# Performance work log

Measured on AMD Instinct MI355X. Metric: run time of the kernel, lower is better.

The kernel has to match this reference:

```python
import jax, jax.numpy as jnp
import numpy as np

EPS = 1e-5  # BatchNorm3d default eps


def conv1x1(x, w, b):
    # x: (b, cin, t, h, w); w: (cout, cin); b: (cout,)
    return jnp.einsum('bcthw,oc->bothw', x, w) + b[None, :, None, None, None]


def batchnorm(x):
    # BatchNorm3d(affine=False), training mode: per-channel batch stats over (B,T,H,W)
    mean = jnp.mean(x, axis=(0, 2, 3, 4), keepdims=True)
    var = jnp.var(x, axis=(0, 2, 3, 4), keepdims=True)
    return (x - mean) * jax.lax.rsqrt(var + EPS)


def setup_inputs() -> dict:
    key = jax.random.key(0)
    ks = jax.random.split(key, 9)
    B, C, T, H, W = 4, 512, 16, 14, 14
    IC = C // 4
    s_in = 1.0 / np.sqrt(C)
    s_up = 1.0 / np.sqrt(IC)
    return {
        'maps':    jax.random.normal(ks[0], (B, C, T, H, W), jnp.float32),
        'w_theta': jax.random.uniform(ks[1], (IC, C), jnp.float32, -s_in, s_in),
        'b_theta': jax.random.uniform(ks[2], (IC,),   jnp.float32, -s_in, s_in),
        'w_phalt': jax.random.uniform(ks[3], (IC, C), jnp.float32, -s_in, s_in),
        'b_phalt': jax.random.uniform(ks[4], (IC,),   jnp.float32, -s_in, s_in),
        'w_glob':  jax.random.uniform(ks[5], (IC, C), jnp.float32, -s_in, s_in),
        'b_glob':  jax.random.uniform(ks[6], (IC,),   jnp.float32, -s_in, s_in),
        'w_up':    jax.random.uniform(ks[7], (C, IC), jnp.float32, -s_up, s_up),
        'b_up':    jax.random.uniform(ks[8], (C,),    jnp.float32, -s_up, s_up),
    }


def reference(maps, w_theta, b_theta, w_phalt, b_phalt, w_glob, b_glob, w_up, b_up):
    b, c, t, h, w = maps.shape
    ic = c // 4
    n = t * h * w

    theta_maps = batchnorm(conv1x1(maps, w_theta, b_theta))   # (b, ic, t, h, w)
    phalt_maps = batchnorm(conv1x1(maps, w_phalt, b_phalt))   # computed but UNUSED (bug in original)
    global_maps = batchnorm(conv1x1(maps, w_glob, b_glob))

    theta_x = theta_maps.reshape(b, ic, n)                    # (b, ic, n)
    # NOTE: original code uses theta_maps for phalt_x (faithful to source bug)
    relation = jnp.einsum('bcn,bcm->bnm', theta_x, theta_x)   # (b, n, n)
    relation_normalize = jax.nn.softmax(relation / n, axis=-1)

    global_x = global_maps.reshape(b, ic, n)                  # (b, ic, n)
    y = jnp.einsum('bnm,bcm->bcn', relation_normalize, global_x)
    y = y.reshape(b, ic, t, h, w)

    out = conv1x1(y, w_up, b_up) + maps
    return out
```

## Files before the change

kernel.cpp:

```cpp
#include <hip/hip_runtime.h>
#include <hip/hip_bf16.h>


typedef __attribute__((ext_vector_type(8))) short bf16x8;
typedef __attribute__((ext_vector_type(4))) float f32x4;
typedef __attribute__((ext_vector_type(16))) float f32x16;
typedef __attribute__((ext_vector_type(4))) short s16x4;

#define NTOK 3136
#define NELEM 1605632
#define NSPLIT 4

__device__ inline float bf2f(short u) {
    union { unsigned int i; float f; } v;
    v.i = ((unsigned int)(unsigned short)u) << 16;
    return v.f;
}
__device__ inline short f2bf(float x) {
    union { float f; unsigned int i; } v;
    v.f = x;
    unsigned int r = v.i + 0x7FFFu + ((v.i >> 16) & 1u);
    return (short)(r >> 16);
}
__device__ inline unsigned pk2(float lo, float hi) {
    union { float f; unsigned u; } a, b;
    a.f = lo; b.f = hi;
    return __builtin_amdgcn_perm(b.u, a.u, 0x07060302u);
}
__device__ inline void pl32swap(unsigned &a, unsigned &b) {
    asm("v_permlane32_swap_b32 %0, %1" : "+v"(a), "+v"(b));
}
__device__ inline void glds16(const void* g, void* l) {
    __builtin_amdgcn_global_load_lds((const __attribute__((address_space(1))) void*)g,
                                     (__attribute__((address_space(3))) void*)l, 16, 0, 0);
}

__global__ __launch_bounds__(256) void prep_w(const float* __restrict__ wt,
                                              const float* __restrict__ wg,
                                              const float* __restrict__ wup,
                                              short* __restrict__ Wb,
                                              short* __restrict__ wupb)
{
    const int i = blockIdx.x * 256 + threadIdx.x;
    if (i < 131072) {
        const int r = i >> 9;
        const int c = i & 511;
        const float w = (r < 128) ? wt[(size_t)r * 512 + c] : wg[(size_t)(r - 128) * 512 + c];
        Wb[i] = f2bf(w);
    } else {
        const int j = i - 131072;
        wupb[j] = f2bf(wup[j]);
    }
}

__global__ __launch_bounds__(256) void conv_in_f(const float* __restrict__ maps,
                                                 const short* __restrict__ Wb,
                                                 short* __restrict__ Tt,
                                                 short* __restrict__ Gpre,
                                                 float* __restrict__ psum,
                                                 float* __restrict__ psq)
{
    const int nt = blockIdx.x, b = blockIdx.y;
    const int n0 = nt * 32;
    const int t = threadIdx.x;
    const int w = __builtin_amdgcn_readfirstlane(t >> 6);
    const int lane = t & 63;
    const int l15 = lane & 15, lhi = lane >> 4;

    __shared__ short Bt[32][136];

    const float* mp = maps + (size_t)b * 512 * NTOK + n0;
    const int cl = t >> 3;
    const int f4 = t & 7;

    f32x4 acc[4][2];
#pragma unroll
    for (int g = 0; g < 4; g++)
#pragma unroll
        for (int j = 0; j < 2; j++) acc[g][j] = f32x4{0.f, 0.f, 0.f, 0.f};

    f32x4 rg[4];
#pragma unroll
    for (int p = 0; p < 4; p++)
        rg[p] = *(const f32x4*)(mp + (size_t)(p * 32 + cl) * NTOK + f4 * 4);

    for (int kc = 0; kc < 4; kc++) {
        __syncthreads();
#pragma unroll
        for (int p = 0; p < 4; p++) {
            const int cc = p * 32 + cl;
#pragma unroll
            for (int i = 0; i < 4; i++) Bt[f4 * 4 + i][cc] = f2bf(rg[p][i]);
        }
        if (kc < 3) {
#pragma unroll
            for (int p = 0; p < 4; p++)
                rg[p] = *(const f32x4*)(mp + (size_t)((kc + 1) * 128 + p * 32 + cl) * NTOK + f4 * 4);
        }
        __syncthreads();
#pragma unroll
        for (int ks = 0; ks < 4; ks++) {
            bf16x8 af[4], bv[2];
#pragma unroll
            for (int g = 0; g < 4; g++)
                af[g] = *(const bf16x8*)(Wb + (size_t)(w * 64 + g * 16 + l15) * 512 + kc * 128 + ks * 32 + lhi * 8);
#pragma unroll
            for (int j = 0; j < 2; j++)
                bv[j] = *(const bf16x8*)(&Bt[j * 16 + l15][ks * 32 + lhi * 8]);
#pragma unroll
            for (int g = 0; g < 4; g++)
#pragma unroll
                for (int j = 0; j < 2; j++)
                    acc[g][j] = __builtin_amdgcn_mfma_f32_16x16x32_bf16(af[g], bv[j], acc[g][j], 0, 0, 0);
        }
    }

    if (w < 2) {
#pragma unroll
        for (int g = 0; g < 4; g++)
#pragma unroll
            for (int j = 0; j < 2; j++) {
                s16x4 v;
#pragma unroll
                for (int r = 0; r < 4; r++) v[r] = f2bf(acc[g][j][r]);
                *(s16x4*)(Tt + ((size_t)b * NTOK + n0 + j * 16 + l15) * 128 + w * 64 + g * 16 + lhi * 4) = v;
            }
    } else {
#pragma unroll
        for (int g = 0; g < 4; g++)
#pragma unroll
            for (int j = 0; j < 2; j++)
#pragma unroll
                for (int r = 0; r < 4; r++) {
                    const int icg = (w - 2) * 64 + g * 16 + lhi * 4 + r;
                    Gpre[((size_t)b * 128 + icg) * NTOK + n0 + j * 16 + l15] = f2bf(acc[g][j][r]);
                }
    }
#pragma unroll
    for (int g = 0; g < 4; g++)
#pragma unroll
        for (int r = 0; r < 4; r++) {
            float s = acc[g][0][r] + acc[g][1][r];
            float q = acc[g][0][r] * acc[g][0][r] + acc[g][1][r] * acc[g][1][r];
#pragma unroll
            for (int off = 1; off < 16; off <<= 1) {
                s += __shfl_xor(s, off);
                q += __shfl_xor(q, off);
            }
            if (l15 == 0) {
                const int ch = w * 64 + g * 16 + lhi * 4 + r;
                psum[(size_t)ch * 392 + b * 98 + nt] = s;
                psq [(size_t)ch * 392 + b * 98 + nt] = q;
            }
        }
}

__global__ __launch_bounds__(64) void stats_fin(const float* __restrict__ psum,
                                                const float* __restrict__ psq,
                                                float* __restrict__ st)
{
    const int ch = blockIdx.x;
    const int lane = threadIdx.x;
    float s = 0.f, q = 0.f;
    for (int i = lane; i < 392; i += 64) {
        s += psum[(size_t)ch * 392 + i];
        q += psq [(size_t)ch * 392 + i];
    }
#pragma unroll
    for (int off = 32; off; off >>= 1) { s += __shfl_xor(s, off); q += __shfl_xor(q, off); }
    if (lane == 0) {
        const float mean = s / 12544.f;
        const float var = q / 12544.f - mean * mean;
        st[ch] = mean;
        st[256 + ch] = rsqrtf(var + 1e-5f);
    }
}

__global__ __launch_bounds__(256, 2) void attn_k(const short* __restrict__ Tt,
                                                 const short* __restrict__ Gpre,
                                                 const float* __restrict__ st,
                                                 short* __restrict__ Opart,
                                                 float* __restrict__ dpart)
{
    constexpr int N = NTOK;
    const int b = blockIdx.y, s = blockIdx.z;
    const int w = __builtin_amdgcn_readfirstlane(threadIdx.x >> 6);
    const int lane = threadIdx.x & 63;
    const int l31 = lane & 31, hi = lane >> 5;
    const int q0w = blockIdx.x * 128 + w * 32;

    __shared__ __align__(16) short Kl[2][64][128];
    __shared__ __align__(16) short Vl[2][128][64];

    const short* tb = Tt + (size_t)b * N * 128;
    const short* gb = Gpre + (size_t)b * 128 * N;

    const float kexp = 1.44269504089f / (float)N;
    bf16x8 qf[8];
    {
        int row = q0w + l31; row = row < N ? row : N - 1;
        const short* qp = tb + (size_t)row * 128;
#pragma unroll
        for (int ks = 0; ks < 8; ks++) {
            const int c0 = ks * 16 + hi * 8;
            const bf16x8 v = *(const bf16x8*)(qp + c0);
            const f32x4 mA = *(const f32x4*)(st + c0);
            const f32x4 mB = *(const f32x4*)(st + c0 + 4);
            const f32x4 rA = *(const f32x4*)(st + 256 + c0);
            const f32x4 rB = *(const f32x4*)(st + 256 + c0 + 4);
            bf16x8 q;
#pragma unroll
            for (int j = 0; j < 4; j++) q[j] = f2bf((bf2f(v[j]) - mA[j]) * (rA[j] * rA[j] * kexp));
#pragma unroll
            for (int j = 0; j < 4; j++) q[4 + j] = f2bf((bf2f(v[4 + j]) - mB[j]) * (rB[j] * rB[j] * kexp));
            qf[ks] = q;
        }
    }

    f32x16 accv[4];
#pragma unroll
    for (int it = 0; it < 4; it++)
#pragma unroll
        for (int r = 0; r < 16; r++) accv[it][r] = 0.f;
    float denom = 0.f;

    auto STAGE = [&](int bufi, int m0) {
#pragma unroll
        for (int i = 0; i < 4; i++) {
            const int rb = w * 16 + i * 4;
            const int krow = rb + (lane >> 4);
            const int ls = (lane & 15) ^ (krow & 7);
            glds16(tb + (size_t)(m0 + krow) * 128 + ls * 8, (void*)&Kl[bufi][rb][0]);
        }
#pragma unroll
        for (int i = 0; i < 4; i++) {
            const int rb = w * 32 + i * 8;
            const int vrow = rb + (lane >> 3);
            const int ls = (lane & 7) ^ (vrow & 7);
            glds16(gb + (size_t)vrow * N + m0 + ls * 8, (void*)&Vl[bufi][rb][0]);
        }
    };

    const int nt = (49 - s + NSPLIT - 1) / NSPLIT;
    int mt = s;
    STAGE(0, mt * 64);
    __syncthreads();
    int buf = 0;

    const int fr = (l31 & 7) << 4;

    auto mkpa = [&](const f32x16 &sv, bf16x8 *dst) {
        float e[16];
#pragma unroll
        for (int r = 0; r < 16; r++) { e[r] = exp2f(sv[r]); denom += e[r]; }
        unsigned c0 = pk2(e[0], e[1]),  c1 = pk2(e[2], e[3]);
        unsigned c2 = pk2(e[4], e[5]),  c3 = pk2(e[6], e[7]);
        unsigned c4 = pk2(e[8], e[9]),  c5 = pk2(e[10], e[11]);
        unsigned c6 = pk2(e[12], e[13]), c7 = pk2(e[14], e[15]);
        pl32swap(c0, c2); pl32swap(c1, c3); pl32swap(c4, c6); pl32swap(c5, c7);
        union U { unsigned u[4]; bf16x8 v; } f0, f1;
        f0.u[0] = c0; f0.u[1] = c1; f0.u[2] = c2; f0.u[3] = c3;
        f1.u[0] = c4; f1.u[1] = c5; f1.u[2] = c6; f1.u[3] = c7;
        dst[0] = f0.v; dst[1] = f1.v;
    };

    for (int t = 0; t < nt; ++t) {
        if (t + 1 < nt) STAGE(buf ^ 1, (mt + NSPLIT) * 64);

        f32x16 sv0, sv1;
#pragma unroll
        for (int r = 0; r < 16; r++) { sv0[r] = 0.f; sv1[r] = 0.f; }
#pragma unroll
        for (int ks = 0; ks < 8; ks++) {
            const int co = (ks * 32 + hi * 16) ^ fr;
            bf16x8 kf0 = *(const bf16x8*)((const char*)&Kl[buf][l31][0] + co);
            bf16x8 kf1 = *(const bf16x8*)((const char*)&Kl[buf][32 + l31][0] + co);
            sv0 = __builtin_amdgcn_mfma_f32_32x32x16_bf16(kf0, qf[ks], sv0, 0, 0, 0);
            sv1 = __builtin_amdgcn_mfma_f32_32x32x16_bf16(kf1, qf[ks], sv1, 0, 0, 0);
        }

        bf16x8 pa[4];
        mkpa(sv0, &pa[0]);
        mkpa(sv1, &pa[2]);

#pragma unroll
        for (int kp = 0; kp < 4; kp++) {
            const int cv = kp * 32 + hi * 16;
#pragma unroll
            for (int it = 0; it < 4; it++) {
                const int row = it * 32 + l31;
                bf16x8 vf = *(const bf16x8*)((const char*)&Vl[buf][row][0] + (cv ^ fr));
                accv[it] = __builtin_amdgcn_mfma_f32_32x32x16_bf16(pa[kp], vf, accv[it], 0, 0, 0);
            }
        }
        __syncthreads();
        buf ^= 1;
        mt += NSPLIT;
    }

    denom += __shfl_xor(denom, 32);

    short* op = Opart + ((size_t)(s * 4 + b)) * N * 128;
#pragma unroll
    for (int it = 0; it < 4; it++)
#pragma unroll
        for (int r = 0; r < 16; r++) {
            const int n = q0w + (r & 3) + 8 * (r >> 2) + 4 * hi;
            if (n < N) op[(size_t)n * 128 + it * 32 + l31] = f2bf(accv[it][r]);
        }
    if (lane < 32) {
        const int n = q0w + l31;
        if (n < N) dpart[(size_t)(s * 4 + b) * N + n] = denom;
    }
}

__global__ __launch_bounds__(256) void conv_out_f(const short* __restrict__ Opart,
                                                  const float* __restrict__ dpart,
                                                  const float* __restrict__ st,
                                                  const short* __restrict__ wupb,
                                                  const float* __restrict__ bup,
                                                  const float* __restrict__ maps,
                                                  float* __restrict__ out)
{
    const int n0 = blockIdx.x * 32, b = blockIdx.y;
    const int t = threadIdx.x;

    __shared__ float denl[32];
    __shared__ __align__(16) short Yl[32][128];

    if (t < 32) {
        float d = 0.f;
#pragma unroll
        for (int s = 0; s < NSPLIT; s++) d += dpart[(size_t)(s * 4 + b) * NTOK + n0 + t];
        denl[t] = 1.0f / d;
    }
    __syncthreads();

#pragma unroll
    for (int g = 0; g < 2; g++) {
        const int e = t + g * 256;
        const int nl = e >> 4, icg = (e & 15) * 8;
        const float rdn = denl[nl];
        float sum[8] = {0.f, 0.f, 0.f, 0.f, 0.f, 0.f, 0.f, 0.f};
#pragma unroll
        for (int s = 0; s < NSPLIT; s++) {
            const size_t base = ((size_t)(s * 4 + b) * NTOK + n0 + nl) * 128 + icg;
            const bf16x8 a = *(const bf16x8*)(Opart + base);
#pragma unroll
            for (int j = 0; j < 8; j++) sum[j] += bf2f(a[j]);
        }
        const f32x4 mA = *(const f32x4*)(st + 128 + icg);
        const f32x4 mB = *(const f32x4*)(st + 128 + icg + 4);
        const f32x4 rA = *(const f32x4*)(st + 384 + icg);
        const f32x4 rB = *(const f32x4*)(st + 384 + icg + 4);
        s16x4 v0, v1;
#pragma unroll
        for (int j = 0; j < 4; j++) v0[j] = f2bf((sum[j] * rdn - mA[j]) * rA[j]);
#pragma unroll
        for (int j = 0; j < 4; j++) v1[j] = f2bf((sum[4 + j] * rdn - mB[j]) * rB[j]);
        char* ybase = (char*)&Yl[nl][0];
        const int sw = (nl & 7) << 4;
        *(s16x4*)(ybase + ((icg * 2) ^ sw)) = v0;
        *(s16x4*)(ybase + (((icg * 2) ^ sw) + 8)) = v1;
    }
    __syncthreads();

    const int wv = __builtin_amdgcn_readfirstlane(t >> 6);
    const int lane = t & 63;
    const int l15 = lane & 15, lhi = lane >> 4;
    const int c0 = wv * 128;
    const int fY = (l15 & 7) << 4;

    f32x4 acc[8][2];
#pragma unroll
    for (int g = 0; g < 8; g++)
#pragma unroll
        for (int j = 0; j < 2; j++) acc[g][j] = f32x4{0.f, 0.f, 0.f, 0.f};

#pragma unroll
    for (int ks = 0; ks < 4; ks++) {
        bf16x8 af[8], bv[2];
#pragma unroll
        for (int g = 0; g < 8; g++)
            af[g] = *(const bf16x8*)(wupb + (size_t)(c0 + g * 16 + l15) * 128 + ks * 32 + lhi * 8);
#pragma unroll
        for (int j = 0; j < 2; j++)
            bv[j] = *(const bf16x8*)((const char*)&Yl[j * 16 + l15][0] + ((ks * 64 + lhi * 16) ^ fY));
#pragma unroll
        for (int g = 0; g < 8; g++)
#pragma unroll
            for (int j = 0; j < 2; j++)
                acc[g][j] = __builtin_amdgcn_mfma_f32_16x16x32_bf16(af[g], bv[j], acc[g][j], 0, 0, 0);
    }
#pragma unroll
    for (int g = 0; g < 8; g++)
#pragma unroll
        for (int j = 0; j < 2; j++)
#pragma unroll
            for (int r = 0; r < 4; r++) {
                const int c = c0 + g * 16 + lhi * 4 + r;
                const int n = n0 + j * 16 + l15;
                const size_t o = ((size_t)b * 512 + c) * NTOK + n;
                out[o] = acc[g][j][r] + bup[c] + maps[o];
            }
}

extern "C" void kernel_launch(void* const* d_in, const int* in_sizes, int n_in,
                              void* d_out, int out_size, void* d_ws, size_t ws_size,
                              hipStream_t stream)
{
    const float* maps    = (const float*)d_in[0];
    const float* w_theta = (const float*)d_in[1];
    const float* w_glob  = (const float*)d_in[5];
    const float* w_up    = (const float*)d_in[7];
    const float* b_up    = (const float*)d_in[8];
    float* out = (float*)d_out;

    short* Tt    = (short*)d_ws;
    short* Gpre  = Tt + NELEM;
    short* Wb    = Gpre + NELEM;
    short* wupb  = Wb + 131072;
    float* st    = (float*)(wupb + 65536);
    float* psum  = st + 512;
    float* psq   = psum + 100352;
    float* dpart = psq + 100352;
    short* Opart = (short*)(dpart + 50176);

    prep_w    <<<768,             256, 0, stream>>>(w_theta, w_glob, w_up, Wb, wupb);
    conv_in_f <<<dim3(98, 4),     256, 0, stream>>>(maps, Wb, Tt, Gpre, psum, psq);
    stats_fin <<<256,             64,  0, stream>>>(psum, psq, st);
    attn_k    <<<dim3(25, 4, NSPLIT), 256, 0, stream>>>(Tt, Gpre, st, Opart, dpart);
    conv_out_f<<<dim3(98, 4),     256, 0, stream>>>(Opart, dpart, st, wupb, b_up, maps, out);
}
```

Measured before the change: 89.31 us.

## Remap attention grid to 1D with XCD-aware block placement and split QK accumulators

The attention launch becomes a flat 400-block grid. Block indices are decoded so that blocks sharing the same batch and split, and so the same K/V tiles, tend to land on the same XCD, which should improve L2 reuse on the multi-die GPU. The QK^T MFMA chain is also split into two independent accumulators per tile, shortening the dependency chain so more MFMAs can be in flight, at the cost of extra accumulator registers and an add before exp2.

```diff
diff --git a/kernel.cpp b/kernel.cpp
--- a/kernel.cpp
+++ b/kernel.cpp
@@ -183,11 +183,16 @@
                                                  float* __restrict__ dpart)
 {
     constexpr int N = NTOK;
-    const int b = blockIdx.y, s = blockIdx.z;
+    const int L = blockIdx.x;
+    const int slot = L >> 3;
+    const int hi25 = (slot >= 25) ? 1 : 0;
+    const int pr = (L & 7) + 8 * hi25;
+    const int qb = slot - 25 * hi25;
+    const int b = pr & 3, s = pr >> 2;
     const int w = __builtin_amdgcn_readfirstlane(threadIdx.x >> 6);
     const int lane = threadIdx.x & 63;
     const int l31 = lane & 31, hi = lane >> 5;
-    const int q0w = blockIdx.x * 128 + w * 32;
+    const int q0w = qb * 128 + w * 32;
 
     __shared__ __align__(16) short Kl[2][64][128];
     __shared__ __align__(16) short Vl[2][128][64];
@@ -249,10 +254,10 @@
 
     const int fr = (l31 & 7) << 4;
 
-    auto mkpa = [&](const f32x16 &sv, bf16x8 *dst) {
+    auto mkpa = [&](const f32x16 &sa, const f32x16 &sb, bf16x8 *dst) {
         float e[16];
 #pragma unroll
-        for (int r = 0; r < 16; r++) { e[r] = exp2f(sv[r]); denom += e[r]; }
+        for (int r = 0; r < 16; r++) { e[r] = exp2f(sa[r] + sb[r]); denom += e[r]; }
         unsigned c0 = pk2(e[0], e[1]),  c1 = pk2(e[2], e[3]);
         unsigned c2 = pk2(e[4], e[5]),  c3 = pk2(e[6], e[7]);
         unsigned c4 = pk2(e[8], e[9]),  c5 = pk2(e[10], e[11]);
@@ -267,21 +272,26 @@
     for (int t = 0; t < nt; ++t) {
         if (t + 1 < nt) STAGE(buf ^ 1, (mt + NSPLIT) * 64);
 
-        f32x16 sv0, sv1;
-#pragma unroll
-        for (int r = 0; r < 16; r++) { sv0[r] = 0.f; sv1[r] = 0.f; }
-#pragma unroll
-        for (int ks = 0; ks < 8; ks++) {
-            const int co = (ks * 32 + hi * 16) ^ fr;
-            bf16x8 kf0 = *(const bf16x8*)((const char*)&Kl[buf][l31][0] + co);
-            bf16x8 kf1 = *(const bf16x8*)((const char*)&Kl[buf][32 + l31][0] + co);
-            sv0 = __builtin_amdgcn_mfma_f32_32x32x16_bf16(kf0, qf[ks], sv0, 0, 0, 0);
-            sv1 = __builtin_amdgcn_mfma_f32_32x32x16_bf16(kf1, qf[ks], sv1, 0, 0, 0);
+        f32x16 s0a, s0b, s1a, s1b;
+#pragma unroll
+        for (int r = 0; r < 16; r++) { s0a[r] = 0.f; s0b[r] = 0.f; s1a[r] = 0.f; s1b[r] = 0.f; }
+#pragma unroll
+        for (int ks = 0; ks < 4; ks++) {
+            const int coA = (ks * 32 + hi * 16) ^ fr;
+            const int coB = ((ks + 4) * 32 + hi * 16) ^ fr;
+            bf16x8 k0a = *(const bf16x8*)((const char*)&Kl[buf][l31][0] + coA);
+            bf16x8 k1a = *(const bf16x8*)((const char*)&Kl[buf][32 + l31][0] + coA);
+            bf16x8 k0b = *(const bf16x8*)((const char*)&Kl[buf][l31][0] + coB);
+            bf16x8 k1b = *(const bf16x8*)((const char*)&Kl[buf][32 + l31][0] + coB);
+            s0a = __builtin_amdgcn_mfma_f32_32x32x16_bf16(k0a, qf[ks], s0a, 0, 0, 0);
+            s1a = __builtin_amdgcn_mfma_f32_32x32x16_bf16(k1a, qf[ks], s1a, 0, 0, 0);
+            s0b = __builtin_amdgcn_mfma_f32_32x32x16_bf16(k0b, qf[ks + 4], s0b, 0, 0, 0);
+            s1b = __builtin_amdgcn_mfma_f32_32x32x16_bf16(k1b, qf[ks + 4], s1b, 0, 0, 0);
         }
 
         bf16x8 pa[4];
-        mkpa(sv0, &pa[0]);
-        mkpa(sv1, &pa[2]);
+        mkpa(s0a, s0b, &pa[0]);
+        mkpa(s1a, s1b, &pa[2]);
 
 #pragma unroll
         for (int kp = 0; kp < 4; kp++) {
@@ -426,9 +436,9 @@
     float* dpart = psq + 100352;
     short* Opart = (short*)(dpart + 50176);
 
-    prep_w    <<<768,             256, 0, stream>>>(w_theta, w_glob, w_up, Wb, wupb);
-    conv_in_f <<<dim3(98, 4),     256, 0, stream>>>(maps, Wb, Tt, Gpre, psum, psq);
-    stats_fin <<<256,             64,  0, stream>>>(psum, psq, st);
-    attn_k    <<<dim3(25, 4, NSPLIT), 256, 0, stream>>>(Tt, Gpre, st, Opart, dpart);
-    conv_out_f<<<dim3(98, 4),     256, 0, stream>>>(Opart, dpart, st, wupb, b_up, maps, out);
-}
+    prep_w    <<<768,          256, 0, stream>>>(w_theta, w_glob, w_up, Wb, wupb);
+    conv_in_f <<<dim3(98, 4),  256, 0, stream>>>(maps, Wb, Tt, Gpre, psum, psq);
+    stats_fin <<<256,          64,  0, stream>>>(psum, psq, st);
+    attn_k    <<<400,          256, 0, stream>>>(Tt, Gpre, st, Opart, dpart);
+    conv_out_f<<<dim3(98, 4),  256, 0, stream>>>(Opart, dpart, st, wupb, b_up, maps, out);
+}
```

Measured after the change: 90.23 us. About the same (+1.0%).

## Fuse all stages into one persistent kernel with grid-wide atomic barriers

Applied to the files above, without the earlier changes.

Replaces five separate kernel launches with one persistent kernel of 512 blocks. Each block loops over the work units of every stage, and the stages are separated by software grid barriers built on atomic counters. This removes launch gaps and per-kernel ramp-up and tail costs. In exchange it needs every block to be co-resident (64KB LDS at 2 blocks per CU), adds a memset and spin-wait overhead, and raises LDS use for the small stages.

```diff
diff --git a/kernel.cpp b/kernel.cpp
--- a/kernel.cpp
+++ b/kernel.cpp
@@ -35,39 +35,37 @@
                                      (__attribute__((address_space(3))) void*)l, 16, 0, 0);
 }
 
-__global__ __launch_bounds__(256) void prep_w(const float* __restrict__ wt,
-                                              const float* __restrict__ wg,
-                                              const float* __restrict__ wup,
-                                              short* __restrict__ Wb,
-                                              short* __restrict__ wupb)
-{
-    const int i = blockIdx.x * 256 + threadIdx.x;
-    if (i < 131072) {
-        const int r = i >> 9;
-        const int c = i & 511;
-        const float w = (r < 128) ? wt[(size_t)r * 512 + c] : wg[(size_t)(r - 128) * 512 + c];
-        Wb[i] = f2bf(w);
-    } else {
-        const int j = i - 131072;
-        wupb[j] = f2bf(wup[j]);
-    }
-}
-
-__global__ __launch_bounds__(256) void conv_in_f(const float* __restrict__ maps,
-                                                 const short* __restrict__ Wb,
-                                                 short* __restrict__ Tt,
-                                                 short* __restrict__ Gpre,
-                                                 float* __restrict__ psum,
-                                                 float* __restrict__ psq)
-{
-    const int nt = blockIdx.x, b = blockIdx.y;
+__device__ inline void ggate(int* f) {
+    __syncthreads();
+    if (threadIdx.x == 0) {
+        __threadfence();
+        __hip_atomic_fetch_add(f, 1, __ATOMIC_ACQ_REL, __HIP_MEMORY_SCOPE_AGENT);
+        while (__hip_atomic_load(f, __ATOMIC_ACQUIRE, __HIP_MEMORY_SCOPE_AGENT)
+               < (int)gridDim.x) {
+            __builtin_amdgcn_s_sleep(8);
+        }
+        __threadfence();
+    }
+    __syncthreads();
+}
+
+__device__ __forceinline__ void conv_in_unit(int unit,
+                                             const float* __restrict__ maps,
+                                             const short* __restrict__ Wb,
+                                             short* __restrict__ Tt,
+                                             short* __restrict__ Gpre,
+                                             float* __restrict__ psum,
+                                             float* __restrict__ psq,
+                                             char* lds)
+{
+    const int nt = unit % 98, b = unit / 98;
     const int n0 = nt * 32;
     const int t = threadIdx.x;
     const int w = __builtin_amdgcn_readfirstlane(t >> 6);
     const int lane = t & 63;
     const int l15 = lane & 15, lhi = lane >> 4;
 
-    __shared__ short Bt[32][136];
+    short (*Bt)[136] = (short(*)[136])lds;
 
     const float* mp = maps + (size_t)b * 512 * NTOK + n0;
     const int cl = t >> 3;
@@ -155,42 +153,54 @@
         }
 }
 
-__global__ __launch_bounds__(64) void stats_fin(const float* __restrict__ psum,
-                                                const float* __restrict__ psq,
-                                                float* __restrict__ st)
-{
-    const int ch = blockIdx.x;
-    const int lane = threadIdx.x;
+__device__ __forceinline__ void stats_unit(int ch,
+                                           const float* __restrict__ psum,
+                                           const float* __restrict__ psq,
+                                           float* __restrict__ st,
+                                           char* lds)
+{
+    const int t = threadIdx.x;
     float s = 0.f, q = 0.f;
-    for (int i = lane; i < 392; i += 64) {
+    for (int i = t; i < 392; i += 256) {
         s += psum[(size_t)ch * 392 + i];
         q += psq [(size_t)ch * 392 + i];
     }
 #pragma unroll
     for (int off = 32; off; off >>= 1) { s += __shfl_xor(s, off); q += __shfl_xor(q, off); }
-    if (lane == 0) {
-        const float mean = s / 12544.f;
-        const float var = q / 12544.f - mean * mean;
+    float* ls = (float*)lds;
+    const int w = t >> 6;
+    __syncthreads();
+    if ((t & 63) == 0) { ls[w] = s; ls[4 + w] = q; }
+    __syncthreads();
+    if (t == 0) {
+        float S = ls[0] + ls[1] + ls[2] + ls[3];
+        float Q = ls[4] + ls[5] + ls[6] + ls[7];
+        const float mean = S / 12544.f;
+        const float var = Q / 12544.f - mean * mean;
         st[ch] = mean;
         st[256 + ch] = rsqrtf(var + 1e-5f);
     }
 }
 
-__global__ __launch_bounds__(256, 2) void attn_k(const short* __restrict__ Tt,
-                                                 const short* __restrict__ Gpre,
-                                                 const float* __restrict__ st,
-                                                 short* __restrict__ Opart,
-                                                 float* __restrict__ dpart)
+__device__ __forceinline__ void attn_unit(int u,
+                                          const short* __restrict__ Tt,
+                                          const short* __restrict__ Gpre,
+                                          const float* __restrict__ st,
+                                          short* __restrict__ Opart,
+                                          float* __restrict__ dpart,
+                                          char* lds)
 {
     constexpr int N = NTOK;
-    const int b = blockIdx.y, s = blockIdx.z;
+    const int qb = u % 25;
+    const int rem = u / 25;
+    const int b = rem & 3, s = rem >> 2;
     const int w = __builtin_amdgcn_readfirstlane(threadIdx.x >> 6);
     const int lane = threadIdx.x & 63;
     const int l31 = lane & 31, hi = lane >> 5;
-    const int q0w = blockIdx.x * 128 + w * 32;
-
-    __shared__ __align__(16) short Kl[2][64][128];
-    __shared__ __align__(16) short Vl[2][128][64];
+    const int q0w = qb * 128 + w * 32;
+
+    short (*Kl)[64][128] = (short(*)[64][128])lds;
+    short (*Vl)[128][64] = (short(*)[128][64])(lds + 32768);
 
     const short* tb = Tt + (size_t)b * N * 128;
     const short* gb = Gpre + (size_t)b * 128 * N;
@@ -314,19 +324,21 @@
     }
 }
 
-__global__ __launch_bounds__(256) void conv_out_f(const short* __restrict__ Opart,
-                                                  const float* __restrict__ dpart,
-                                                  const float* __restrict__ st,
-                                                  const short* __restrict__ wupb,
-                                                  const float* __restrict__ bup,
-                                                  const float* __restrict__ maps,
-                                                  float* __restrict__ out)
-{
-    const int n0 = blockIdx.x * 32, b = blockIdx.y;
+__device__ __forceinline__ void conv_out_unit(int unit,
+                                              const short* __restrict__ Opart,
+                                              const float* __restrict__ dpart,
+                                              const float* __restrict__ st,
+                                              const short* __restrict__ wupb,
+                                              const float* __restrict__ bup,
+                                              const float* __restrict__ maps,
+                                              float* __restrict__ out,
+                                              char* lds)
+{
+    const int n0 = (unit % 98) * 32, b = unit / 98;
     const int t = threadIdx.x;
 
-    __shared__ float denl[32];
-    __shared__ __align__(16) short Yl[32][128];
+    float* denl = (float*)lds;
+    short (*Yl)[128] = (short(*)[128])(lds + 128);
 
     if (t < 32) {
         float d = 0.f;
@@ -403,6 +415,52 @@
                 const size_t o = ((size_t)b * 512 + c) * NTOK + n;
                 out[o] = acc[g][j][r] + bup[c] + maps[o];
             }
+}
+
+__global__ __launch_bounds__(256, 2) void fused_all(const float* maps,
+                                                    const float* wt,
+                                                    const float* wg,
+                                                    const float* wup,
+                                                    const float* bup,
+                                                    short* Tt, short* Gpre,
+                                                    short* Wb, short* wupb,
+                                                    float* st, float* psum,
+                                                    float* psq, float* dpart,
+                                                    short* Opart, float* out,
+                                                    int* flags)
+{
+    __shared__ __align__(16) char lds[65536];
+    const int nb = gridDim.x;
+    const int bid = blockIdx.x;
+
+    for (int u = bid; u < 768; u += nb) {
+        const int i = u * 256 + threadIdx.x;
+        if (i < 131072) {
+            const int r = i >> 9;
+            const int c = i & 511;
+            const float wv = (r < 128) ? wt[(size_t)r * 512 + c] : wg[(size_t)(r - 128) * 512 + c];
+            Wb[i] = f2bf(wv);
+        } else {
+            const int j = i - 131072;
+            wupb[j] = f2bf(wup[j]);
+        }
+    }
+    ggate(&flags[0]);
+
+    for (int u = bid; u < 392; u += nb)
+        conv_in_unit(u, maps, Wb, Tt, Gpre, psum, psq, lds);
+    ggate(&flags[1]);
+
+    for (int u = bid; u < 256; u += nb)
+        stats_unit(u, psum, psq, st, lds);
+    ggate(&flags[2]);
+
+    for (int u = bid; u < 400; u += nb)
+        attn_unit(u, Tt, Gpre, st, Opart, dpart, lds);
+    ggate(&flags[3]);
+
+    for (int u = bid; u < 392; u += nb)
+        conv_out_unit(u, Opart, dpart, st, wupb, bup, maps, out, lds);
 }
 
 extern "C" void kernel_launch(void* const* d_in, const int* in_sizes, int n_in,
@@ -425,10 +483,10 @@
     float* psq   = psum + 100352;
     float* dpart = psq + 100352;
     short* Opart = (short*)(dpart + 50176);
-
-    prep_w    <<<768,             256, 0, stream>>>(w_theta, w_glob, w_up, Wb, wupb);
-    conv_in_f <<<dim3(98, 4),     256, 0, stream>>>(maps, Wb, Tt, Gpre, psum, psq);
-    stats_fin <<<256,             64,  0, stream>>>(psum, psq, st);
-    attn_k    <<<dim3(25, 4, NSPLIT), 256, 0, stream>>>(Tt, Gpre, st, Opart, dpart);
-    conv_out_f<<<dim3(98, 4),     256, 0, stream>>>(Opart, dpart, st, wupb, b_up, maps, out);
-}
+    int*   flags = (int*)(Opart + (size_t)NSPLIT * NELEM);
+
+    hipMemsetAsync(flags, 0, 4 * sizeof(int), stream);
+    fused_all<<<512, 256, 0, stream>>>(maps, w_theta, w_glob, w_up, b_up,
+                                       Tt, Gpre, Wb, wupb, st, psum, psq,
+                                       dpart, Opart, out, flags);
+}
```

Measured after the change: 354.7 us. 297% more time.
